# Kernel optimization log

Hardware: AMD Instinct MI355X
Metric: run time of the kernel (lower is better)

The kernel has to match this reference:

```python
import jax, jax.numpy as jnp
import numpy as np

C_M, C_Z, N_HEADS = 256, 128, 8
HEAD_DIM = C_M // N_HEADS
EPS = 1e-5


def _layer_norm(x, scale, bias):
    mu = jnp.mean(x, axis=-1, keepdims=True)
    var = jnp.mean(jnp.square(x - mu), axis=-1, keepdims=True)
    return (x - mu) * jax.lax.rsqrt(var + EPS) * scale + bias


def setup_inputs() -> dict:
    key = jax.random.key(0)
    ks = jax.random.split(key, 12)
    N, L = 128, 256
    s_m = 1.0 / np.sqrt(C_M)
    s_z = 1.0 / np.sqrt(C_Z)
    return {
        "msa": jax.random.normal(ks[0], (N, L, C_M), dtype=jnp.float32),
        "pair": jax.random.normal(ks[1], (L, L, C_Z), dtype=jnp.float32),
        "ln_m_scale": jnp.ones((C_M,), jnp.float32),
        "ln_m_bias": jnp.zeros((C_M,), jnp.float32),
        "ln_z_scale": jnp.ones((C_Z,), jnp.float32),
        "ln_z_bias": jnp.zeros((C_Z,), jnp.float32),
        "w_q": jax.random.normal(ks[2], (C_M, C_M), jnp.float32) * s_m,
        "w_k": jax.random.normal(ks[3], (C_M, C_M), jnp.float32) * s_m,
        "w_v": jax.random.normal(ks[4], (C_M, C_M), jnp.float32) * s_m,
        "w_b": jax.random.normal(ks[5], (N_HEADS, C_Z), jnp.float32) * s_z,
        "w_out": jax.random.normal(ks[6], (C_M, C_M), jnp.float32) * s_m,
        "b_out": jnp.zeros((C_M,), jnp.float32),
        "w_gate": jax.random.normal(ks[7], (C_M, C_M), jnp.float32) * s_m,
        "b_gate": jnp.zeros((C_M,), jnp.float32),
    }


def reference(msa, pair, ln_m_scale, ln_m_bias, ln_z_scale, ln_z_bias,
              w_q, w_k, w_v, w_b, w_out, b_out, w_gate, b_gate):
    N, L, _ = msa.shape
    m = _layer_norm(msa, ln_m_scale, ln_m_bias)          # (N, L, c_m)
    z = _layer_norm(pair, ln_z_scale, ln_z_bias)         # (L, L, c_z)
    q = (m @ w_q.T).reshape(N, L, N_HEADS, HEAD_DIM)
    k = (m @ w_k.T).reshape(N, L, N_HEADS, HEAD_DIM)
    v = (m @ w_v.T).reshape(N, L, N_HEADS, HEAD_DIM)
    attn = jnp.einsum('bihd,bjhd->bhij', q, k) / np.sqrt(HEAD_DIM).astype(np.float32)
    bias = jnp.einsum('ijc,hc->hij', z, w_b)             # (H, L, L)
    attn = jax.nn.softmax(attn + bias[None], axis=-1)    # (N, H, L, L)
    out = jnp.einsum('bhij,bjhd->bihd', attn, v).reshape(N, L, C_M)
    return msa + jax.nn.sigmoid(m @ w_gate.T + b_gate) * (out @ w_out.T + b_out)
```

## Files before the change

### kernel.cpp

```cpp
#include <hip/hip_runtime.h>

typedef unsigned short u16;
typedef float f32x4 __attribute__((ext_vector_type(4)));
typedef __bf16 bf16x8 __attribute__((ext_vector_type(8)));

__device__ __forceinline__ u16 f2bf(float f) {
  union { float f; unsigned u; } v; v.f = f;
  unsigned r = (v.u + 0x7fffu + ((v.u >> 16) & 1u)) >> 16;
  return (u16)r;
}
__device__ __forceinline__ float bf2f(u16 h) {
  union { unsigned u; float f; } v; v.u = ((unsigned)h) << 16; return v.f;
}

#define GLOAD16(gp, lp)                                                        \
  __builtin_amdgcn_global_load_lds(                                            \
      (const __attribute__((address_space(1))) void*)(gp),                     \
      (__attribute__((address_space(3))) void*)(lp), 16, 0, 0)

#define LOG2E 1.4426950408889634f
#define HS 1048576

__global__ __launch_bounds__(256) void pre_kernel(
    const float* __restrict__ x, const float* __restrict__ sc,
    const float* __restrict__ bi, u16* __restrict__ mo,
    const float* __restrict__ wq, const float* __restrict__ wk,
    const float* __restrict__ wv, const float* __restrict__ wg,
    const float* __restrict__ wo, u16* __restrict__ wfrag, u16* __restrict__ wobf,
    const float* __restrict__ pair, const float* __restrict__ scz,
    const float* __restrict__ biz, const float* __restrict__ wb,
    u16* __restrict__ biasQ)
{
  __shared__ float swc[1024];
  __shared__ float sA[8], sB2[8];
  const int tid = threadIdx.x;

  if (blockIdx.x < 8192) {
    const int row  = blockIdx.x * 4 + (tid >> 6);
    const int lane = tid & 63;
    const float4 v = *(const float4*)(x + (size_t)row * 256 + lane * 4);
    float s = v.x + v.y + v.z + v.w;
    #pragma unroll
    for (int off = 1; off < 64; off <<= 1) s += __shfl_xor(s, off);
    const float mu = s * 0.00390625f;
    const float d0 = v.x - mu, d1 = v.y - mu, d2 = v.z - mu, d3 = v.w - mu;
    float vs = d0*d0 + d1*d1 + d2*d2 + d3*d3;
    #pragma unroll
    for (int off = 1; off < 64; off <<= 1) vs += __shfl_xor(vs, off);
    const float rstd = rsqrtf(vs * 0.00390625f + 1e-5f);
    const float4 scv = *(const float4*)(sc + lane * 4);
    const float4 biv = *(const float4*)(bi + lane * 4);
    ushort4 o;
    o.x = f2bf(d0 * rstd * scv.x + biv.x);
    o.y = f2bf(d1 * rstd * scv.y + biv.y);
    o.z = f2bf(d2 * rstd * scv.z + biv.z);
    o.w = f2bf(d3 * rstd * scv.w + biv.w);
    *(ushort4*)(mo + (size_t)row * 256 + lane * 4) = o;
  } else if (blockIdx.x < 9216) {
    const int d4 = (blockIdx.x - 8192) * 256 + tid;
    const int e0 = (d4 & 1) * 4;
    const int lane = (d4 >> 1) & 63;
    const int n  = (d4 >> 7) & 1;
    const int W  = (d4 >> 8) & 3;
    const int kk = (d4 >> 10) & 7;
    const int h  = (d4 >> 13) & 7;
    const float* src = (W == 0) ? wq : (W == 1) ? wk : (W == 2) ? wv : wg;
    const int row = h * 32 + n * 16 + (lane & 15);
    const int col = kk * 32 + (lane >> 4) * 8 + e0;
    float4 v = *(const float4*)(src + (size_t)row * 256 + col);
    ushort4 o;
    o.x = f2bf(v.x); o.y = f2bf(v.y); o.z = f2bf(v.z); o.w = f2bf(v.w);
    *(ushort4*)(wfrag + ((((((size_t)h * 8 + kk) * 4 + W) * 2 + n) * 64 + lane) * 8 + e0)) = o;
  } else if (blockIdx.x < 9280) {
    int e = ((blockIdx.x - 9216) * 256 + tid) * 4;
    int row = e >> 8, col = e & 255;
    float4 v = *(const float4*)(wo + (size_t)row * 256 + col);
    ushort4 o;
    o.x = f2bf(v.x); o.y = f2bf(v.y); o.z = f2bf(v.z); o.w = f2bf(v.w);
    *(ushort4*)(wobf + e) = o;
  } else {
    #pragma unroll
    for (int k = 0; k < 4; ++k) {
      int idx = k * 256 + tid;
      int c = idx >> 3, h = idx & 7;
      swc[idx] = scz[c] * wb[h * 128 + c];
    }
    __syncthreads();
    if (tid < 8) {
      float a = 0.f, b2 = 0.f;
      for (int c = 0; c < 128; ++c) {
        a  += swc[c * 8 + tid];
        b2 += biz[c] * wb[tid * 128 + c];
      }
      sA[tid] = a; sB2[tid] = b2;
    }
    __syncthreads();
    const int gt = (blockIdx.x - 9280) * 256 + tid;
    const int ij = gt >> 1, hg = gt & 1;
    const float* xr = pair + (size_t)ij * 128;
    float s = 0.f, ss = 0.f;
    float d0 = 0.f, d1 = 0.f, d2 = 0.f, d3 = 0.f;
    for (int c0 = 0; c0 < 128; c0 += 4) {
      float4 xv4 = *(const float4*)(xr + c0);
      float xe[4] = {xv4.x, xv4.y, xv4.z, xv4.w};
      #pragma unroll
      for (int e = 0; e < 4; ++e) {
        const float xv = xe[e];
        s += xv; ss += xv * xv;
        const f32x4 wv = *(const f32x4*)&swc[(c0 + e) * 8 + hg * 4];
        d0 += xv * wv[0]; d1 += xv * wv[1];
        d2 += xv * wv[2]; d3 += xv * wv[3];
      }
    }
    const float mu = s * 0.0078125f;
    const float rstd = rsqrtf(ss * 0.0078125f - mu * mu + 1e-5f);
    const int i = ij >> 8, j = ij & 255;
    const float dd[4] = {d0, d1, d2, d3};
    #pragma unroll
    for (int hh = 0; hh < 4; ++hh) {
      const int h = hg * 4 + hh;
      const float bias = (dd[hh] - mu * sA[h]) * rstd + sB2[h];
      biasQ[h * 65536 + i * 256 + j] = f2bf(bias * LOG2E);
    }
  }
}

__global__ __launch_bounds__(512) void qkv_attn_kernel(
    const u16* __restrict__ A, const u16* __restrict__ wfrag,
    const float* __restrict__ bgate, const u16* __restrict__ biasQ,
    u16* __restrict__ gatebh, u16* __restrict__ attn_oh)
{
  __shared__ u16 Qlds[256 * 40];
  __shared__ u16 Klds[256 * 40];
  __shared__ u16 sVt[32 * 264];
  const int tid = threadIdx.x, lane = tid & 63, w = tid >> 6;
  const int g = lane >> 4, r15 = lane & 15;
  const int h = blockIdx.x & 7;
  const int b = blockIdx.x >> 3;
  const size_t rowbase = (size_t)b * 256;

  bf16x8 af[2][8];
  #pragma unroll
  for (int m = 0; m < 2; ++m) {
    const size_t arow = rowbase + w * 32 + m * 16 + r15;
    #pragma unroll
    for (int kk = 0; kk < 8; ++kk)
      af[m][kk] = *(const bf16x8*)(A + arow * 256 + kk * 32 + g * 8);
  }

  const u16* wfh = wfrag + (size_t)h * 32768;

  #define PROJ(Wi, ACC)                                                        \
    {                                                                          \
      _Pragma("unroll")                                                        \
      for (int m = 0; m < 2; ++m)                                              \
        _Pragma("unroll")                                                      \
        for (int n = 0; n < 2; ++n) ACC[m][n] = (f32x4){0.f, 0.f, 0.f, 0.f};   \
      _Pragma("unroll")                                                        \
      for (int kk = 0; kk < 8; ++kk) {                                         \
        bf16x8 wf0 = *(const bf16x8*)(wfh + ((kk * 4 + Wi) * 2 + 0) * 512 + lane * 8); \
        bf16x8 wf1 = *(const bf16x8*)(wfh + ((kk * 4 + Wi) * 2 + 1) * 512 + lane * 8); \
        _Pragma("unroll")                                                      \
        for (int m = 0; m < 2; ++m) {                                          \
          ACC[m][0] = __builtin_amdgcn_mfma_f32_16x16x32_bf16(wf0, af[m][kk], ACC[m][0], 0, 0, 0); \
          ACC[m][1] = __builtin_amdgcn_mfma_f32_16x16x32_bf16(wf1, af[m][kk], ACC[m][1], 0, 0, 0); \
        }                                                                      \
      }                                                                        \
    }

  f32x4 acc[2][2];

  PROJ(0, acc);
  #pragma unroll
  for (int m = 0; m < 2; ++m)
    #pragma unroll
    for (int n = 0; n < 2; ++n) {
      ushort4 o;
      o.x = f2bf(acc[m][n][0] * (0.17677669529663687f * LOG2E));
      o.y = f2bf(acc[m][n][1] * (0.17677669529663687f * LOG2E));
      o.z = f2bf(acc[m][n][2] * (0.17677669529663687f * LOG2E));
      o.w = f2bf(acc[m][n][3] * (0.17677669529663687f * LOG2E));
      *(ushort4*)&Qlds[(w * 32 + m * 16 + r15) * 40 + n * 16 + g * 4] = o;
    }

  PROJ(1, acc);
  #pragma unroll
  for (int m = 0; m < 2; ++m)
    #pragma unroll
    for (int n = 0; n < 2; ++n) {
      ushort4 o;
      o.x = f2bf(acc[m][n][0]); o.y = f2bf(acc[m][n][1]);
      o.z = f2bf(acc[m][n][2]); o.w = f2bf(acc[m][n][3]);
      *(ushort4*)&Klds[(w * 32 + m * 16 + r15) * 40 + n * 16 + g * 4] = o;
    }

  PROJ(2, acc);
  #pragma unroll
  for (int m = 0; m < 2; ++m) {
    const int pos = (w >> 1) * 64 + (w & 1) * 32 + (r15 >> 2) * 8 + m * 4 + (r15 & 3);
    #pragma unroll
    for (int n = 0; n < 2; ++n)
      #pragma unroll
      for (int jj = 0; jj < 4; ++jj)
        sVt[(n * 16 + g * 4 + jj) * 264 + pos] = f2bf(acc[m][n][jj]);
  }

  PROJ(3, acc);
  ushort4 gpk[2][2];
  {
    #pragma unroll
    for (int m = 0; m < 2; ++m)
      #pragma unroll
      for (int n = 0; n < 2; ++n) {
        const f32x4 gb = *(const f32x4*)(bgate + h * 32 + n * 16 + g * 4);
        gpk[m][n].x = f2bf(1.0f / (1.0f + __expf(-(acc[m][n][0] + gb[0]))));
        gpk[m][n].y = f2bf(1.0f / (1.0f + __expf(-(acc[m][n][1] + gb[1]))));
        gpk[m][n].z = f2bf(1.0f / (1.0f + __expf(-(acc[m][n][2] + gb[2]))));
        gpk[m][n].w = f2bf(1.0f / (1.0f + __expf(-(acc[m][n][3] + gb[3]))));
      }
  }
  __syncthreads();

  const int qrel0 = w * 32 + r15;
  bf16x8 qf[2];
  #pragma unroll
  for (int m = 0; m < 2; ++m)
    qf[m] = *(const bf16x8*)&Qlds[(qrel0 + m * 16) * 40 + g * 8];

  f32x4 oacc[2][2] = {};
  float lrun[2] = {0.f, 0.f};
  const u16* biasH = biasQ + (size_t)h * 65536;

  ushort4 bvu[2][4];
  #pragma unroll
  for (int m = 0; m < 2; ++m)
    #pragma unroll
    for (int n = 0; n < 4; ++n)
      bvu[m][n] = *(const ushort4*)(biasH + (size_t)(qrel0 + m * 16) * 256 + n * 16 + g * 4);

  for (int jb = 0; jb < 4; ++jb) {
    bf16x8 kf[4];
    #pragma unroll
    for (int n = 0; n < 4; ++n)
      kf[n] = *(const bf16x8*)&Klds[(jb * 64 + n * 16 + r15) * 40 + g * 8];
    f32x4 s[2][4];
    __builtin_amdgcn_s_setprio(1);
    #pragma unroll
    for (int m = 0; m < 2; ++m) {
      #pragma unroll
      for (int n = 0; n < 4; ++n) {
        f32x4 z = {0.f, 0.f, 0.f, 0.f};
        s[m][n] = __builtin_amdgcn_mfma_f32_16x16x32_bf16(kf[n], qf[m], z, 0, 0, 0);
      }
    }
    __builtin_amdgcn_s_setprio(0);
    #pragma unroll
    for (int m = 0; m < 2; ++m) {
      #pragma unroll
      for (int n = 0; n < 4; ++n) {
        const u16* bb = (const u16*)&bvu[m][n];
        #pragma unroll
        for (int rr = 0; rr < 4; ++rr) s[m][n][rr] += bf2f(bb[rr]);
      }
    }
    if (jb < 3) {
      const int j1 = jb + 1;
      #pragma unroll
      for (int m = 0; m < 2; ++m)
        #pragma unroll
        for (int n = 0; n < 4; ++n)
          bvu[m][n] = *(const ushort4*)(biasH + (size_t)(qrel0 + m * 16) * 256 + j1 * 64 + n * 16 + g * 4);
    }
    #pragma unroll
    for (int m = 0; m < 2; ++m)
      #pragma unroll
      for (int n = 0; n < 4; ++n)
        #pragma unroll
        for (int rr = 0; rr < 4; ++rr) {
          float p = __builtin_amdgcn_exp2f(s[m][n][rr]);
          s[m][n][rr] = p;
          lrun[m] += p;
        }
    #pragma unroll
    for (int kb = 0; kb < 2; ++kb) {
      bf16x8 vt[2];
      #pragma unroll
      for (int nd = 0; nd < 2; ++nd)
        vt[nd] = *(const bf16x8*)&sVt[(nd * 16 + r15) * 264 + jb * 64 + kb * 32 + g * 8];
      __builtin_amdgcn_s_setprio(1);
      #pragma unroll
      for (int m = 0; m < 2; ++m) {
        bf16x8 pv;
        #pragma unroll
        for (int rr = 0; rr < 4; ++rr) {
          pv[rr]     = (__bf16)s[m][2 * kb][rr];
          pv[4 + rr] = (__bf16)s[m][2 * kb + 1][rr];
        }
        #pragma unroll
        for (int nd = 0; nd < 2; ++nd)
          oacc[m][nd] = __builtin_amdgcn_mfma_f32_16x16x32_bf16(pv, vt[nd], oacc[m][nd], 0, 0, 0);
      }
      __builtin_amdgcn_s_setprio(0);
    }
  }

  #pragma unroll
  for (int m = 0; m < 2; ++m) {
    float l = lrun[m];
    l += __shfl_xor(l, 16);
    l += __shfl_xor(l, 32);
    const float inv = 1.0f / l;
    #pragma unroll
    for (int rr = 0; rr < 4; ++rr) {
      const float invq = __shfl(inv, g * 4 + rr);
      const size_t qrow = rowbase + w * 32 + m * 16 + g * 4 + rr;
      #pragma unroll
      for (int nd = 0; nd < 2; ++nd)
        attn_oh[(size_t)h * HS + qrow * 32 + nd * 16 + r15] = f2bf(oacc[m][nd][rr] * invq);
    }
  }

  #pragma unroll
  for (int m = 0; m < 2; ++m) {
    const size_t grow = rowbase + w * 32 + m * 16 + r15;
    #pragma unroll
    for (int n = 0; n < 2; ++n)
      *(ushort4*)(gatebh + (size_t)h * HS + grow * 32 + n * 16 + g * 4) = gpk[m][n];
  }
}

__global__ __launch_bounds__(512, 2) void gemm_epi1(
    const u16* __restrict__ attn_oh, const u16* __restrict__ B,
    const u16* __restrict__ gatebh, float* __restrict__ Cf,
    const float* __restrict__ msa, const float* __restrict__ bout)
{
  __shared__ u16 sB[64 * 256];
  const int tid = threadIdx.x, lane = tid & 63, w = tid >> 6;
  const int g = lane >> 4, r15 = lane & 15;
  const int x = blockIdx.x & 7;
  const int j = blockIdx.x >> 3;
  const int cg = j & 3;
  const int rpl = j >> 2;
  const int bcol = cg * 64;

  #pragma unroll
  for (int i = 0; i < 4; ++i) {
    int c = i * 512 + tid;
    int col = c >> 5, s = c & 31;
    int lc = (s & 24) | ((s ^ col) & 7);
    GLOAD16(B + (size_t)(bcol + col) * 256 + lc * 8, &sB[c * 8]);
  }

  float bo[4];
  #pragma unroll
  for (int n = 0; n < 4; ++n) bo[n] = bout[bcol + n * 16 + r15];

  const size_t brow = ((size_t)(x * 16) + rpl) * 256;
  bf16x8 af[2][8];
  #pragma unroll
  for (int m = 0; m < 2; ++m) {
    const size_t arow = brow + w * 32 + m * 16 + r15;
    #pragma unroll
    for (int kk = 0; kk < 8; ++kk)
      af[m][kk] = *(const bf16x8*)(attn_oh + (size_t)kk * HS + arow * 32 + g * 8);
  }
  __syncthreads();

  f32x4 acc[2][4] = {};
  #pragma unroll
  for (int kk = 0; kk < 8; ++kk) {
    bf16x8 bfr[4];
    #pragma unroll
    for (int n = 0; n < 4; ++n) {
      int col = n * 16 + r15;
      int lcq = kk * 4 + g;
      int s = (lcq & 24) | ((lcq ^ col) & 7);
      bfr[n] = *(const bf16x8*)&sB[col * 256 + s * 8];
    }
    #pragma unroll
    for (int m = 0; m < 2; ++m)
      #pragma unroll
      for (int n = 0; n < 4; ++n)
        acc[m][n] = __builtin_amdgcn_mfma_f32_16x16x32_bf16(af[m][kk], bfr[n], acc[m][n], 0, 0, 0);
  }

  #pragma unroll
  for (int m = 0; m < 2; ++m) {
    const int row0 = (int)brow + w * 32 + m * 16 + g * 4;
    #pragma unroll
    for (int n = 0; n < 4; ++n) {
      const int col = bcol + n * 16 + r15;
      #pragma unroll
      for (int rr = 0; rr < 4; ++rr) {
        float v = acc[m][n][rr] + bo[n];
        const size_t orow = (size_t)(row0 + rr);
        float gg = bf2f(gatebh[(size_t)(col >> 5) * HS + orow * 32 + (col & 31)]);
        Cf[orow * 256 + col] = msa[orow * 256 + col] + gg * v;
      }
    }
  }
}

extern "C" void kernel_launch(void* const* d_in, const int* in_sizes, int n_in,
                              void* d_out, int out_size, void* d_ws, size_t ws_size,
                              hipStream_t stream)
{
  (void)in_sizes; (void)n_in; (void)out_size; (void)ws_size;
  const float* msa        = (const float*)d_in[0];
  const float* pair       = (const float*)d_in[1];
  const float* ln_m_scale = (const float*)d_in[2];
  const float* ln_m_bias  = (const float*)d_in[3];
  const float* ln_z_scale = (const float*)d_in[4];
  const float* ln_z_bias  = (const float*)d_in[5];
  const float* w_q        = (const float*)d_in[6];
  const float* w_k        = (const float*)d_in[7];
  const float* w_v        = (const float*)d_in[8];
  const float* w_b        = (const float*)d_in[9];
  const float* w_out      = (const float*)d_in[10];
  const float* b_out      = (const float*)d_in[11];
  const float* w_gate     = (const float*)d_in[12];
  const float* b_gate     = (const float*)d_in[13];

  char* ws = (char*)d_ws;
  u16*   m_bf    = (u16*)(ws);
  u16*   wobf    = (u16*)(ws + 16777216);
  u16*   wfrag   = (u16*)(ws + 16908288);
  u16*   gatebh  = (u16*)(ws + 17432576);
  u16*   biasQ   = (u16*)(ws + 34209792);
  u16*   attn_oh = (u16*)(ws + 35258368);
  float* out = (float*)d_out;

  pre_kernel<<<dim3(9792), dim3(256), 0, stream>>>(
      msa, ln_m_scale, ln_m_bias, m_bf, w_q, w_k, w_v, w_gate, w_out, wfrag, wobf,
      pair, ln_z_scale, ln_z_bias, w_b, biasQ);
  qkv_attn_kernel<<<dim3(1024), dim3(512), 0, stream>>>(
      m_bf, wfrag, b_gate, biasQ, gatebh, attn_oh);
  gemm_epi1<<<dim3(512), dim3(512), 0, stream>>>(attn_oh, wobf, gatebh, out, msa, b_out);
}
```

Measured before the change: 128.7 us.

## Fuse MSA layer norm into the QKV attention kernel's operand load

Removes the separate MSA layer-norm pass from the preprocessing kernel, which used to write a bf16 normalized copy to workspace. The attention kernel now reads the fp32 msa rows directly, computes mean and variance per row with a single-pass sum/sum-of-squares reduction across lanes, and normalizes into bf16 fragments in registers. This removes a full write and re-read of the normalized activation. In exchange, each of the eight per-head blocks reads the fp32 rows twice and redoes the normalization, and the variance formula is less numerically stable.

```diff
diff --git a/kernel.cpp b/kernel.cpp
--- a/kernel.cpp
+++ b/kernel.cpp
@@ -22,8 +22,6 @@
 #define HS 1048576
 
 __global__ __launch_bounds__(256) void pre_kernel(
-    const float* __restrict__ x, const float* __restrict__ sc,
-    const float* __restrict__ bi, u16* __restrict__ mo,
     const float* __restrict__ wq, const float* __restrict__ wk,
     const float* __restrict__ wv, const float* __restrict__ wg,
     const float* __restrict__ wo, u16* __restrict__ wfrag, u16* __restrict__ wobf,
@@ -35,29 +33,8 @@
   __shared__ float sA[8], sB2[8];
   const int tid = threadIdx.x;
 
-  if (blockIdx.x < 8192) {
-    const int row  = blockIdx.x * 4 + (tid >> 6);
-    const int lane = tid & 63;
-    const float4 v = *(const float4*)(x + (size_t)row * 256 + lane * 4);
-    float s = v.x + v.y + v.z + v.w;
-    #pragma unroll
-    for (int off = 1; off < 64; off <<= 1) s += __shfl_xor(s, off);
-    const float mu = s * 0.00390625f;
-    const float d0 = v.x - mu, d1 = v.y - mu, d2 = v.z - mu, d3 = v.w - mu;
-    float vs = d0*d0 + d1*d1 + d2*d2 + d3*d3;
-    #pragma unroll
-    for (int off = 1; off < 64; off <<= 1) vs += __shfl_xor(vs, off);
-    const float rstd = rsqrtf(vs * 0.00390625f + 1e-5f);
-    const float4 scv = *(const float4*)(sc + lane * 4);
-    const float4 biv = *(const float4*)(bi + lane * 4);
-    ushort4 o;
-    o.x = f2bf(d0 * rstd * scv.x + biv.x);
-    o.y = f2bf(d1 * rstd * scv.y + biv.y);
-    o.z = f2bf(d2 * rstd * scv.z + biv.z);
-    o.w = f2bf(d3 * rstd * scv.w + biv.w);
-    *(ushort4*)(mo + (size_t)row * 256 + lane * 4) = o;
-  } else if (blockIdx.x < 9216) {
-    const int d4 = (blockIdx.x - 8192) * 256 + tid;
+  if (blockIdx.x < 256) {
+    const int d4 = blockIdx.x * 256 + tid;
     const int e0 = (d4 & 1) * 4;
     const int lane = (d4 >> 1) & 63;
     const int n  = (d4 >> 7) & 1;
@@ -71,8 +48,8 @@
     ushort4 o;
     o.x = f2bf(v.x); o.y = f2bf(v.y); o.z = f2bf(v.z); o.w = f2bf(v.w);
     *(ushort4*)(wfrag + ((((((size_t)h * 8 + kk) * 4 + W) * 2 + n) * 64 + lane) * 8 + e0)) = o;
-  } else if (blockIdx.x < 9280) {
-    int e = ((blockIdx.x - 9216) * 256 + tid) * 4;
+  } else if (blockIdx.x < 320) {
+    int e = ((blockIdx.x - 256) * 256 + tid) * 4;
     int row = e >> 8, col = e & 255;
     float4 v = *(const float4*)(wo + (size_t)row * 256 + col);
     ushort4 o;
@@ -95,7 +72,7 @@
       sA[tid] = a; sB2[tid] = b2;
     }
     __syncthreads();
-    const int gt = (blockIdx.x - 9280) * 256 + tid;
+    const int gt = (blockIdx.x - 320) * 256 + tid;
     const int ij = gt >> 1, hg = gt & 1;
     const float* xr = pair + (size_t)ij * 128;
     float s = 0.f, ss = 0.f;
@@ -126,7 +103,8 @@
 }
 
 __global__ __launch_bounds__(512) void qkv_attn_kernel(
-    const u16* __restrict__ A, const u16* __restrict__ wfrag,
+    const float* __restrict__ msa, const float* __restrict__ lnsc,
+    const float* __restrict__ lnbi, const u16* __restrict__ wfrag,
     const float* __restrict__ bgate, const u16* __restrict__ biasQ,
     u16* __restrict__ gatebh, u16* __restrict__ attn_oh)
 {
@@ -139,13 +117,54 @@
   const int b = blockIdx.x >> 3;
   const size_t rowbase = (size_t)b * 256;
 
+  const float* xr0 = msa + (rowbase + w * 32 + r15) * 256;
+  const float* xr1 = xr0 + 16 * 256;
+  float s1[2] = {0.f, 0.f}, s2[2] = {0.f, 0.f};
+  #pragma unroll
+  for (int kk = 0; kk < 8; ++kk) {
+    const int c0 = kk * 32 + g * 8;
+    const float4 a0 = *(const float4*)(xr0 + c0);
+    const float4 a1 = *(const float4*)(xr0 + c0 + 4);
+    const float4 b0 = *(const float4*)(xr1 + c0);
+    const float4 b1 = *(const float4*)(xr1 + c0 + 4);
+    s1[0] += a0.x + a0.y + a0.z + a0.w + a1.x + a1.y + a1.z + a1.w;
+    s2[0] += a0.x*a0.x + a0.y*a0.y + a0.z*a0.z + a0.w*a0.w
+           + a1.x*a1.x + a1.y*a1.y + a1.z*a1.z + a1.w*a1.w;
+    s1[1] += b0.x + b0.y + b0.z + b0.w + b1.x + b1.y + b1.z + b1.w;
+    s2[1] += b0.x*b0.x + b0.y*b0.y + b0.z*b0.z + b0.w*b0.w
+           + b1.x*b1.x + b1.y*b1.y + b1.z*b1.z + b1.w*b1.w;
+  }
+  float aS[2], bS[2];
+  #pragma unroll
+  for (int m = 0; m < 2; ++m) {
+    float s = s1[m]; s += __shfl_xor(s, 16); s += __shfl_xor(s, 32);
+    float q = s2[m]; q += __shfl_xor(q, 16); q += __shfl_xor(q, 32);
+    const float mu = s * 0.00390625f;
+    const float rstd = rsqrtf(q * 0.00390625f - mu * mu + 1e-5f);
+    aS[m] = rstd; bS[m] = -mu * rstd;
+  }
+  asm volatile("" ::: "memory");
+
   bf16x8 af[2][8];
   #pragma unroll
-  for (int m = 0; m < 2; ++m) {
-    const size_t arow = rowbase + w * 32 + m * 16 + r15;
-    #pragma unroll
-    for (int kk = 0; kk < 8; ++kk)
-      af[m][kk] = *(const bf16x8*)(A + arow * 256 + kk * 32 + g * 8);
+  for (int kk = 0; kk < 8; ++kk) {
+    const int c0 = kk * 32 + g * 8;
+    const float4 sc0 = *(const float4*)(lnsc + c0);
+    const float4 sc1 = *(const float4*)(lnsc + c0 + 4);
+    const float4 bi0 = *(const float4*)(lnbi + c0);
+    const float4 bi1 = *(const float4*)(lnbi + c0 + 4);
+    const float se[8] = {sc0.x, sc0.y, sc0.z, sc0.w, sc1.x, sc1.y, sc1.z, sc1.w};
+    const float be[8] = {bi0.x, bi0.y, bi0.z, bi0.w, bi1.x, bi1.y, bi1.z, bi1.w};
+    #pragma unroll
+    for (int m = 0; m < 2; ++m) {
+      const float* xr = (m == 0) ? xr0 : xr1;
+      const float4 a0 = *(const float4*)(xr + c0);
+      const float4 a1 = *(const float4*)(xr + c0 + 4);
+      const float xe[8] = {a0.x, a0.y, a0.z, a0.w, a1.x, a1.y, a1.z, a1.w};
+      #pragma unroll
+      for (int e = 0; e < 8; ++e)
+        af[m][kk][e] = (__bf16)((xe[e] * aS[m] + bS[m]) * se[e] + be[e]);
+    }
   }
 
   const u16* wfh = wfrag + (size_t)h * 32768;
@@ -422,7 +441,6 @@
   const float* b_gate     = (const float*)d_in[13];
 
   char* ws = (char*)d_ws;
-  u16*   m_bf    = (u16*)(ws);
   u16*   wobf    = (u16*)(ws + 16777216);
   u16*   wfrag   = (u16*)(ws + 16908288);
   u16*   gatebh  = (u16*)(ws + 17432576);
@@ -430,10 +448,10 @@
   u16*   attn_oh = (u16*)(ws + 35258368);
   float* out = (float*)d_out;
 
-  pre_kernel<<<dim3(9792), dim3(256), 0, stream>>>(
-      msa, ln_m_scale, ln_m_bias, m_bf, w_q, w_k, w_v, w_gate, w_out, wfrag, wobf,
+  pre_kernel<<<dim3(832), dim3(256), 0, stream>>>(
+      w_q, w_k, w_v, w_gate, w_out, wfrag, wobf,
       pair, ln_z_scale, ln_z_bias, w_b, biasQ);
   qkv_attn_kernel<<<dim3(1024), dim3(512), 0, stream>>>(
-      m_bf, wfrag, b_gate, biasQ, gatebh, attn_oh);
+      msa, ln_m_scale, ln_m_bias, wfrag, b_gate, biasQ, gatebh, attn_oh);
   gemm_epi1<<<dim3(512), dim3(512), 0, stream>>>(attn_oh, wobf, gatebh, out, msa, b_out);
 }
```

Result: slower. 168.8 us (+31.2%).
